# Kernel tuning notes

Hardware: AMD Instinct MI355X
Metric: run time of the kernel (lower is better)

Reference implementation:

```python
import jax, jax.numpy as jnp
import numpy as np
import math

V, L, D, H, S_MAX = 32000, 6, 768, 8, 256
HD = D // H
SCALE_FACTOR = 2  # attn_scale_factor in the original (TUPE-style)
POS_SCALING = float(HD * SCALE_FACTOR) ** (-0.5)
REL_BINS, MAX_DIST = 32, 128


def _rel_pos_bucket_np(rel, num_buckets=REL_BINS, max_distance=MAX_DIST):
    # bidirectional T5-style bucketing (faithful to relative_position_bucket)
    n = -rel
    num_buckets //= 2
    ret = (n < 0).astype(np.int64) * num_buckets
    n = np.abs(n)
    max_exact = num_buckets // 2
    is_small = n < max_exact
    val_if_large = max_exact + (
        np.log(np.maximum(n, 1).astype(np.float32) / max_exact)
        / math.log(max_distance / max_exact) * (num_buckets - max_exact)
    ).astype(np.int64)
    val_if_large = np.minimum(val_if_large, num_buckets - 1)
    ret += np.where(is_small, n, val_if_large)
    return ret


def _layernorm(x, g, b, eps=1e-5):
    mu = jnp.mean(x, axis=-1, keepdims=True)
    var = jnp.var(x, axis=-1, keepdims=True)
    return (x - mu) * jax.lax.rsqrt(var + eps) * g + b


def setup_inputs() -> dict:
    key = jax.random.key(0)
    ks = jax.random.split(key, 16)
    B, S = 32, 256
    init = lambda k, shape: (jax.random.normal(k, shape, jnp.float32) * 0.02)
    pos_idx = np.arange(S)
    rp = _rel_pos_bucket_np(pos_idx[None, :] - pos_idx[:, None])  # [S,S]
    return {
        "tokens": jax.random.randint(ks[0], (B, S), 0, V, dtype=jnp.int32),
        "embed_tokens": init(ks[1], (V, D)),
        "pos_emb": init(ks[2], (S_MAX + 1, D)),
        "pos_q_w": init(ks[3], (D, D)), "pos_q_b": jnp.zeros((D,), jnp.float32),
        "pos_k_w": init(ks[4], (D, D)), "pos_k_b": jnp.zeros((D,), jnp.float32),
        "pos_ln_g": jnp.ones((D,), jnp.float32), "pos_ln_b": jnp.zeros((D,), jnp.float32),
        "rel_bias_table": init(ks[5], (REL_BINS + 1, H)),
        "rp_bucket": jnp.asarray(rp, jnp.int32),
        "Wq": init(ks[6], (L, D, D)), "bq": jnp.zeros((L, D), jnp.float32),
        "Wk": init(ks[7], (L, D, D)), "bk": jnp.zeros((L, D), jnp.float32),
        "Wv": init(ks[8], (L, D, D)), "bv": jnp.zeros((L, D), jnp.float32),
        "Wo": init(ks[9], (L, D, D)), "bo": jnp.zeros((L, D), jnp.float32),
    }


def reference(tokens, embed_tokens, pos_emb, pos_q_w, pos_q_b, pos_k_w, pos_k_b,
              pos_ln_g, pos_ln_b, rel_bias_table, rp_bucket,
              Wq, bq, Wk, bk, Wv, bv, Wo, bo):
    B, S = tokens.shape
    # relative positional bias: bucket lookup -> [H,S,S]
    rel_bias = rel_bias_table[rp_bucket]            # [S,S,H]
    rel_bias = jnp.transpose(rel_bias, (2, 0, 1))   # [H,S,S]
    # absolute positional bias (TUPE): LN(pos) -> per-head q/k -> bmm
    w = _layernorm(pos_emb[:S], pos_ln_g, pos_ln_b)             # [S,D]
    pq = (w @ pos_q_w.T + pos_q_b).reshape(S, H, HD) * POS_SCALING
    pk = (w @ pos_k_w.T + pos_k_b).reshape(S, H, HD)
    abs_bias = jnp.einsum('ihd,jhd->hij', pq, pk)               # [H,S,S]
    bias = (abs_bias + rel_bias)[None]                          # [1,H,S,S]

    x = embed_tokens[tokens]                                    # [B,S,D]
    scale = float(HD * SCALE_FACTOR) ** (-0.5)
    for l in range(L):
        q = (x @ Wq[l].T + bq[l]).reshape(B, S, H, HD) * scale
        k = (x @ Wk[l].T + bk[l]).reshape(B, S, H, HD)
        v = (x @ Wv[l].T + bv[l]).reshape(B, S, H, HD)
        scores = jnp.einsum('bihd,bjhd->bhij', q, k) + bias     # [B,H,S,S]
        attn = jax.nn.softmax(scores, axis=-1)
        o = jnp.einsum('bhij,bjhd->bihd', attn, v).reshape(B, S, D)
        x = o @ Wo[l].T + bo[l]
    return x[:, 0, :]  # sentence rep [B,D]
```

## Files before the change

### kernel.cpp

```cpp
#include <hip/hip_runtime.h>
#include <hip/hip_bf16.h>
#include <math.h>

constexpr int SEQ = 256;
constexpr int DIM = 768;
constexpr int NH  = 8;
constexpr int HD  = 96;

typedef __attribute__((ext_vector_type(8))) short short8;
typedef __attribute__((ext_vector_type(4))) float f32x4;
using bf16 = __hip_bfloat16;

#define ASYNC_COPY16(gptr, lptr) \
  __builtin_amdgcn_global_load_lds((const __attribute__((address_space(1))) void*)(gptr), \
                                   (__attribute__((address_space(3))) void*)(lptr), 16, 0, 0)

__global__ __launch_bounds__(256) void gemm_kernel(
    const float* __restrict__ A, int lda, long aoz,
    const float* __restrict__ W, int ldw, long woz,
    const float* __restrict__ bias, long boz,
    bf16* __restrict__ C, int ldc, long coz,
    int M, int N, int K, float scale,
    const int* __restrict__ rp, const float* __restrict__ rtab)
{
    const int hz = blockIdx.z;
    A += (long)hz * aoz;
    W += (long)hz * woz;
    if (bias) bias += (long)hz * boz;
    C += (long)hz * coz;

    __shared__ float As[16][68];
    __shared__ float Ws[16][68];

    const int bm = blockIdx.y * 64;
    const int bn = blockIdx.x * 64;
    const int tid = threadIdx.x;
    const int tx = tid & 15;
    const int ty = tid >> 4;

    float acc[4][4] = {};

    for (int k0 = 0; k0 < K; k0 += 16) {
#pragma unroll
        for (int i = 0; i < 4; i++) {
            int idx = tid + i * 256;
            int r = idx >> 4, c = idx & 15;
            As[c][r] = A[(long)(bm + r) * lda + (k0 + c)];
            Ws[c][r] = W[(long)(bn + r) * ldw + (k0 + c)];
        }
        __syncthreads();
#pragma unroll
        for (int kk = 0; kk < 16; kk++) {
            const float4 a = *(const float4*)&As[kk][ty * 4];
            const float4 w = *(const float4*)&Ws[kk][tx * 4];
            acc[0][0] += a.x * w.x; acc[0][1] += a.x * w.y; acc[0][2] += a.x * w.z; acc[0][3] += a.x * w.w;
            acc[1][0] += a.y * w.x; acc[1][1] += a.y * w.y; acc[1][2] += a.y * w.z; acc[1][3] += a.y * w.w;
            acc[2][0] += a.z * w.x; acc[2][1] += a.z * w.y; acc[2][2] += a.z * w.z; acc[2][3] += a.z * w.w;
            acc[3][0] += a.w * w.x; acc[3][1] += a.w * w.y; acc[3][2] += a.w * w.z; acc[3][3] += a.w * w.w;
        }
        __syncthreads();
    }

    const int n0 = bn + tx * 4;
    float4 bv = make_float4(0.f, 0.f, 0.f, 0.f);
    if (bias) bv = *(const float4*)&bias[n0];
#pragma unroll
    for (int i = 0; i < 4; i++) {
        const int m = bm + ty * 4 + i;
        float4 r;
        if (rtab) {
            r.x = acc[i][0] * scale + rtab[rp[(n0 + 0) * 256 + m] * 8 + hz];
            r.y = acc[i][1] * scale + rtab[rp[(n0 + 1) * 256 + m] * 8 + hz];
            r.z = acc[i][2] * scale + rtab[rp[(n0 + 2) * 256 + m] * 8 + hz];
            r.w = acc[i][3] * scale + rtab[rp[(n0 + 3) * 256 + m] * 8 + hz];
        } else {
            r.x = (acc[i][0] + bv.x) * scale;
            r.y = (acc[i][1] + bv.y) * scale;
            r.z = (acc[i][2] + bv.z) * scale;
            r.w = (acc[i][3] + bv.w) * scale;
        }
        bf16 t4[4];
        t4[0] = __float2bfloat16(r.x);
        t4[1] = __float2bfloat16(r.y);
        t4[2] = __float2bfloat16(r.z);
        t4[3] = __float2bfloat16(r.w);
        *(uint2*)&C[(long)m * ldc + n0] = *(uint2*)t4;
    }
}

constexpr int RB_A = 10368;
constexpr int RB_B = RB_A + 3456;
constexpr int RB_C = RB_B + 54;
constexpr int RB_D = RB_C + 6144;
constexpr int RB_E = RB_D + 256;
constexpr int RB_F = RB_E + 1152;
constexpr int RB_G = RB_F + 2;

__global__ __launch_bounds__(256) void setup_mega_kernel(
    const int* __restrict__ tokens, const float* __restrict__ embed,
    const float* __restrict__ pos_emb,
    const float* __restrict__ pos_q_w, const float* __restrict__ pos_q_b,
    const float* __restrict__ pos_k_w, const float* __restrict__ pos_k_b,
    const float* __restrict__ pos_ln_g, const float* __restrict__ pos_ln_b,
    const float* __restrict__ Wq, const float* __restrict__ Wk,
    const float* __restrict__ Wv, const float* __restrict__ Wo,
    const float* __restrict__ bq, const float* __restrict__ bk,
    const float* __restrict__ bv,
    bf16* __restrict__ wqkv, bf16* __restrict__ woT, float* __restrict__ bqkv,
    bf16* __restrict__ xb, bf16* __restrict__ wln,
    bf16* __restrict__ wsW, float* __restrict__ wsB, float scale)
{
    const int bid = blockIdx.x, tid = threadIdx.x;

    if (bid < RB_A) {
        const long idx = (long)bid * 256 + tid;
        const long e = idx * 4;
        const int k = (int)(e % 768);
        const long nl = e / 768;
        const int n = (int)(nl % 2304);
        const int l = (int)(nl / 2304);
        const float* src;
        float sc = 1.f;
        if (n < 768)       { src = Wq + ((long)l * 768 + n) * 768; sc = scale; }
        else if (n < 1536) { src = Wk + ((long)l * 768 + (n - 768)) * 768; }
        else               { src = Wv + ((long)l * 768 + (n - 1536)) * 768; }
        const float4 v = *(const float4*)&src[k];
        bf16 tmp[4];
        tmp[0] = __float2bfloat16(v.x * sc);
        tmp[1] = __float2bfloat16(v.y * sc);
        tmp[2] = __float2bfloat16(v.z * sc);
        tmp[3] = __float2bfloat16(v.w * sc);
        *(uint2*)&wqkv[((long)l * 2304 + n) * 768 + k] = *(uint2*)tmp;
    } else if (bid < RB_B) {
        __shared__ float t[32][33];
        const int b2 = bid - RB_A;
        const int l = b2 / 576, r2 = b2 % 576;
        const int c0 = (r2 % 24) * 32, j0 = (r2 / 24) * 32;
        const int tx = tid & 31, ty = tid >> 5;
        const float* src = Wo + (long)l * 768 * 768;
#pragma unroll
        for (int rr = 0; rr < 32; rr += 8)
            t[ty + rr][tx] = src[(long)(c0 + ty + rr) * 768 + j0 + tx];
        __syncthreads();
        bf16* dst = woT + (long)l * 768 * 768;
#pragma unroll
        for (int rr = 0; rr < 32; rr += 8)
            dst[(long)(j0 + ty + rr) * 768 + c0 + tx] = __float2bfloat16(t[tx][ty + rr]);
    } else if (bid < RB_C) {
        const int idx = (bid - RB_B) * 256 + tid;
        if (idx < 6 * 2304) {
            const int n = idx % 2304, l = idx / 2304;
            float v;
            if (n < 768)       v = bq[l * 768 + n] * scale;
            else if (n < 1536) v = bk[l * 768 + (n - 768)];
            else               v = bv[l * 768 + (n - 1536)];
            bqkv[idx] = v;
        }
    } else if (bid < RB_D) {
        const int idx = (bid - RB_C) * 256 + tid;
        const int t = idx / 192;
        const int d = idx - t * 192;
        const int tok = tokens[t];
        const float4 v = ((const float4*)(embed + (long)tok * DIM))[d];
        bf16 tmp[4];
        tmp[0] = __float2bfloat16(v.x);
        tmp[1] = __float2bfloat16(v.y);
        tmp[2] = __float2bfloat16(v.z);
        tmp[3] = __float2bfloat16(v.w);
        *(uint2*)&xb[(long)t * DIM + d * 4] = *(uint2*)tmp;
    } else if (bid < RB_E) {
        __shared__ float buf[256];
        const int i = bid - RB_D;
        const float* row = pos_emb + (long)i * DIM;
        float v0 = row[tid], v1 = row[tid + 256], v2 = row[tid + 512];
        buf[tid] = v0 + v1 + v2;
        __syncthreads();
        for (int off = 128; off > 0; off >>= 1) {
            if (tid < off) buf[tid] += buf[tid + off];
            __syncthreads();
        }
        const float mean = buf[0] * (1.f / 768.f);
        __syncthreads();
        const float d0 = v0 - mean, d1 = v1 - mean, d2 = v2 - mean;
        buf[tid] = d0 * d0 + d1 * d1 + d2 * d2;
        __syncthreads();
        for (int off = 128; off > 0; off >>= 1) {
            if (tid < off) buf[tid] += buf[tid + off];
            __syncthreads();
        }
        const float rstd = rsqrtf(buf[0] * (1.f / 768.f) + 1e-5f);
        bf16* wr = wln + (long)i * DIM;
        wr[tid]       = __float2bfloat16(d0 * rstd * pos_ln_g[tid]       + pos_ln_b[tid]);
        wr[tid + 256] = __float2bfloat16(d1 * rstd * pos_ln_g[tid + 256] + pos_ln_b[tid + 256]);
        wr[tid + 512] = __float2bfloat16(d2 * rstd * pos_ln_g[tid + 512] + pos_ln_b[tid + 512]);
    } else if (bid < RB_F) {
        const long idx = (long)(bid - RB_E) * 256 + tid;
        const long e = idx * 4;
        const float4 v = (e < 589824) ? *(const float4*)&pos_q_w[e]
                                      : *(const float4*)&pos_k_w[e - 589824];
        bf16 tmp[4];
        tmp[0] = __float2bfloat16(v.x);
        tmp[1] = __float2bfloat16(v.y);
        tmp[2] = __float2bfloat16(v.z);
        tmp[3] = __float2bfloat16(v.w);
        *(uint2*)&wsW[e] = *(uint2*)tmp;
    } else {
        const int idx = (bid - RB_F) * 256 + tid;
        wsB[idx] = (idx < 768) ? pos_q_b[idx] : pos_k_b[idx - 768];
    }
}

__global__ __launch_bounds__(256) void fused_bias_kernel(
    const bf16* __restrict__ wqkv, const float* __restrict__ bo,
    const float* __restrict__ bqkv, float* __restrict__ bf_)
{
    const int l = blockIdx.y;
    const int lane = threadIdx.x & 63, wave = threadIdx.x >> 6;
    const int nloc = wave * 8 + (lane >> 3);
    const int seg = lane & 7;
    const int n = blockIdx.x * 32 + nloc;
    const bf16* wrow = wqkv + ((long)(l + 1) * 2304 + n) * 768 + seg * 96;
    const float* bsrc = bo + (long)l * 768 + seg * 96;
    float s = 0.f;
#pragma unroll
    for (int c8 = 0; c8 < 12; c8++) {
        const short8 w8 = *(const short8*)&wrow[c8 * 8];
#pragma unroll
        for (int e = 0; e < 8; e++) {
            bf16 b;
            *(short*)&b = w8[e];
            s += __bfloat162float(b) * bsrc[c8 * 8 + e];
        }
    }
    s += __shfl_xor(s, 1);
    s += __shfl_xor(s, 2);
    s += __shfl_xor(s, 4);
    if (seg == 0) bf_[l * 2304 + n] = s + bqkv[(l + 1) * 2304 + n];
}

#define GEMM_PREF(AS, BS, KB)                                                 \
  {                                                                           \
    _Pragma("unroll")                                                         \
    for (int i = 0; i < 2; i++) {                                             \
      const int u = tid + i * 512;                                            \
      const int r = u >> 3, c = u & 7;                                        \
      const int ca = c ^ (r & 7);                                             \
      ASYNC_COPY16(A + (bm + r) * (long)K + (KB) + ca * 8, &AS[u * 8]);       \
      ASYNC_COPY16(B + (bn + r) * (long)K + (KB) + ca * 8, &BS[u * 8]);       \
    }                                                                         \
  }

#define GEMM_COMPUTE(AS, BS)                                                  \
  {                                                                           \
    _Pragma("unroll")                                                         \
    for (int ks = 0; ks < 2; ks++) {                                          \
      const int cc = ks * 4 + quad;                                           \
      short8 af[4], bfr[2];                                                   \
      _Pragma("unroll")                                                       \
      for (int t = 0; t < 4; t++) {                                           \
        const int ra = wm * 64 + t * 16 + col;                                \
        af[t] = *(const short8*)&AS[ra * 64 + ((cc ^ (ra & 7)) * 8)];         \
      }                                                                       \
      _Pragma("unroll")                                                       \
      for (int t = 0; t < 2; t++) {                                           \
        const int rb = wn * 32 + t * 16 + col;                                \
        bfr[t] = *(const short8*)&BS[rb * 64 + ((cc ^ (rb & 7)) * 8)];        \
      }                                                                       \
      _Pragma("unroll")                                                       \
      for (int tm = 0; tm < 4; tm++)                                          \
        _Pragma("unroll")                                                     \
        for (int tn = 0; tn < 2; tn++)                                        \
          acc[tm][tn] = __builtin_amdgcn_mfma_f32_16x16x32_bf16(af[tm], bfr[tn], acc[tm][tn], 0, 0, 0); \
    }                                                                         \
  }

__global__ __launch_bounds__(512, 4) void gemm_bf16_kernel(
    const bf16* __restrict__ A, const bf16* __restrict__ B,
    const float* __restrict__ bias,
    bf16* __restrict__ Cb, bf16* __restrict__ vTout, float* __restrict__ Cf,
    int N, int K, int swz, long az, long bz, long cz, long biasz, int skipQ)
{
    __shared__ bf16 As0[128 * 64];
    __shared__ bf16 Bs0[128 * 64];
    __shared__ bf16 As1[128 * 64];
    __shared__ bf16 Bs1[128 * 64];

    A += (long)blockIdx.z * az;
    B += (long)blockIdx.z * bz;
    if (Cb) Cb += (long)blockIdx.z * cz;
    if (Cf) Cf += (long)blockIdx.z * cz;
    if (bias) bias += (long)blockIdx.z * biasz;

    const int tid = threadIdx.x;
    const int lane = tid & 63, wave = tid >> 6;
    const int wm = wave & 1, wn = wave >> 1;

    int bmt, bnt;
    if (swz) {
        const int id = blockIdx.x + gridDim.x * blockIdx.y;
        const int xcd = id & 7, loc = id >> 3;
        bmt = xcd * 8 + (loc & 7);
        bnt = loc >> 3;
    } else {
        bmt = blockIdx.y;
        bnt = blockIdx.x;
    }
    if (skipQ && bnt < 6 && (bmt & 1)) return;

    const long bm = (long)bmt * 128, bn = (long)bnt * 128;
    const int col = lane & 15, quad = lane >> 4;

    f32x4 acc[4][2] = {};

    GEMM_PREF(As0, Bs0, 0);
    for (int kk = 0; kk < K; kk += 128) {
        __syncthreads();
        GEMM_PREF(As1, Bs1, kk + 64);
        GEMM_COMPUTE(As0, Bs0);
        __syncthreads();
        if (kk + 128 < K) GEMM_PREF(As0, Bs0, kk + 128);
        GEMM_COMPUTE(As1, Bs1);
    }

    const bool toVT = (vTout != nullptr) && (bn >= 1536);

    if (toVT) {
        __syncthreads();
        bf16* tb = (wave < 4 ? As0 : Bs0) + (wave & 3) * 2048;
#pragma unroll
        for (int tn = 0; tn < 2; tn++) {
            const int nl = tn * 16 + col;
            const float bvv = bias[bn + wn * 32 + nl];
#pragma unroll
            for (int tm = 0; tm < 4; tm++) {
                const int mc = tm * 4 + quad;
                bf16 t4[4];
#pragma unroll
                for (int r = 0; r < 4; r++)
                    t4[r] = __float2bfloat16(acc[tm][tn][r] + bvv);
                *(uint2*)&tb[(nl * 16 + (mc ^ (nl & 15))) * 4] = *(uint2*)t4;
            }
        }
        const int b_  = (int)((bm + wm * 64) >> 8);
        const int s0  = (int)((bm + wm * 64) & 255);
        const long nb = bn + wn * 32 - 1536;
#pragma unroll
        for (int it2 = 0; it2 < 8; it2++) {
            const int nl = it2 * 4 + quad;
            const uint2 v = *(const uint2*)&tb[(nl * 16 + (col ^ (nl & 15))) * 4];
            *(uint2*)&vTout[((long)b_ * 768 + nb + nl) * 256 + s0 + col * 4] = v;
        }
    } else if (Cf) {
#pragma unroll
        for (int tn = 0; tn < 2; tn++) {
            const long n = bn + wn * 32 + tn * 16 + col;
            const float bvv = bias ? bias[n] : 0.f;
#pragma unroll
            for (int tm = 0; tm < 4; tm++) {
                const long m0 = bm + wm * 64 + tm * 16 + quad * 4;
#pragma unroll
                for (int r = 0; r < 4; r++)
                    Cf[(m0 + r) * N + n] = acc[tm][tn][r] + bvv;
            }
        }
    } else {
#pragma unroll
        for (int tn = 0; tn < 2; tn++) {
            const long n = bn + wn * 32 + tn * 16 + col;
            const float bvv = bias ? bias[n] : 0.f;
#pragma unroll
            for (int tm = 0; tm < 4; tm++) {
                const long m0 = bm + wm * 64 + tm * 16 + quad * 4;
#pragma unroll
                for (int r = 0; r < 4; r++)
                    Cb[(m0 + r) * N + n] = __float2bfloat16(acc[tm][tn][r] + bvv);
            }
        }
    }
}

#define PREF_K(DST, JC)                                                      \
  { _Pragma("unroll")                                                        \
    for (int i = 0; i < 4; i++) {                                            \
      const int u = tid + i * 256;                                           \
      const int r = u >> 4, pp = u & 15;                                     \
      const int c = pp ^ (r & 15);                                           \
      ASYNC_COPY16(kbase + ((JC) * 64 + r) * 2304 + c * 8, &DST[u * 8]);     \
    } }

#define PREF_V(DST, KC)                                                      \
  { _Pragma("unroll")                                                        \
    for (int i = 0; i < 3; i++) {                                            \
      const int u = tid + i * 256;                                           \
      const int r = u >> 3, pp = u & 7;                                      \
      const int c = pp ^ (r & 7);                                            \
      ASYNC_COPY16(vbase + r * 256 + (KC) * 64 + c * 8, &DST[u * 8]);        \
    } }

#define SCORE(BUF, JC)                                                       \
  { _Pragma("unroll")                                                        \
    for (int ks = 0; ks < 3; ks++) {                                         \
      _Pragma("unroll")                                                      \
      for (int jt2 = 0; jt2 < 4; jt2++) {                                    \
        const int row = jt2 * 16 + col;                                      \
        const int c = ks * 4 + quad;                                         \
        const short8 bk_ = *(const short8*)&BUF[row * 128 + ((c ^ (row & 15)) * 8)]; \
        accS[(JC) * 4 + jt2] = __builtin_amdgcn_mfma_f32_16x16x32_bf16(aq[ks], bk_, accS[(JC) * 4 + jt2], 0, 0, 0); \
      } } }

#define PV(BUF, KC)                                                          \
  { _Pragma("unroll")                                                        \
    for (int k2 = 0; k2 < 2; k2++) {                                         \
      const short8 ap = *(const short8*)&Ps[(wave * 16 + col) * PS + (KC) * 64 + k2 * 32 + quad * 8]; \
      _Pragma("unroll")                                                      \
      for (int nt = 0; nt < 6; nt++) {                                       \
        const int row = nt * 16 + col;                                       \
        const int c = k2 * 4 + quad;                                         \
        const short8 bv_ = *(const short8*)&BUF[row * 64 + ((c ^ (row & 7)) * 8)]; \
        accO[nt] = __builtin_amdgcn_mfma_f32_16x16x32_bf16(ap, bv_, accO[nt], 0, 0, 0); \
      } } }

__global__ __launch_bounds__(256) void attn_mfma_kernel(
    const bf16* __restrict__ qkv, const bf16* __restrict__ vT,
    const bf16* __restrict__ biasT, bf16* __restrict__ o)
{
    constexpr int PS = 264;
    __shared__ bf16 Ps[64 * PS];
    __shared__ bf16 KV0[64 * 128];
    __shared__ bf16 KV1[64 * 128];

    const int blk = blockIdx.x;
    const int b  = blk & 31;
    const int h  = (blk >> 5) & 7;
    const int it = blk >> 8;
    const int i0 = it * 64;
    const int tid = threadIdx.x, lane = tid & 63, wave = tid >> 6;
    const int col = lane & 15, quad = lane >> 4;
    const long rowbase = (long)b * SEQ;

    const bf16* kbase = qkv + rowbase * 2304 + 768 + h * 96;
    const bf16* vbase = vT + ((long)b * 768 + h * 96) * 256;

    PREF_K(KV0, 0);

    short8 aq[3];
    {
        const bf16* qrow = qkv + (rowbase + i0 + wave * 16 + col) * 2304 + h * 96;
#pragma unroll
        for (int ks = 0; ks < 3; ks++)
            aq[ks] = *(const short8*)&qrow[ks * 32 + quad * 8];
    }

    f32x4 accS[16] = {};
    __syncthreads();
    PREF_K(KV1, 1);
    SCORE(KV0, 0);
    __syncthreads();
    PREF_K(KV0, 2);
    SCORE(KV1, 1);
    __syncthreads();
    PREF_K(KV1, 3);
    SCORE(KV0, 2);
    __syncthreads();
    PREF_V(KV0, 0);
    SCORE(KV1, 3);

    const bf16* bbT = biasT + (long)h * SEQ * SEQ + i0 + wave * 16 + quad * 4;
#pragma unroll
    for (int jt = 0; jt < 16; jt++) {
        bf16 b4[4];
        *(uint2*)b4 = *(const uint2*)&bbT[(long)(jt * 16 + col) * SEQ];
        accS[jt][0] += __bfloat162float(b4[0]);
        accS[jt][1] += __bfloat162float(b4[1]);
        accS[jt][2] += __bfloat162float(b4[2]);
        accS[jt][3] += __bfloat162float(b4[3]);
    }

#pragma unroll
    for (int r = 0; r < 4; r++) {
        float m = accS[0][r];
#pragma unroll
        for (int jt = 1; jt < 16; jt++) m = fmaxf(m, accS[jt][r]);
        for (int d = 1; d < 16; d <<= 1) m = fmaxf(m, __shfl_xor(m, d));
        float s = 0.f;
#pragma unroll
        for (int jt = 0; jt < 16; jt++) {
            const float e = __expf(accS[jt][r] - m);
            accS[jt][r] = e;
            s += e;
        }
        for (int d = 1; d < 16; d <<= 1) s += __shfl_xor(s, d);
        const float inv = 1.f / s;
        const int prow = wave * 16 + quad * 4 + r;
#pragma unroll
        for (int jt = 0; jt < 16; jt++)
            Ps[prow * PS + jt * 16 + col] = __float2bfloat16(accS[jt][r] * inv);
    }

    f32x4 accO[6] = {};
    __syncthreads();
    PREF_V(KV1, 1);
    PV(KV0, 0);
    __syncthreads();
    PREF_V(KV0, 2);
    PV(KV1, 1);
    __syncthreads();
    PREF_V(KV1, 3);
    PV(KV0, 2);
    __syncthreads();
    PV(KV1, 3);

#pragma unroll
    for (int nt = 0; nt < 6; nt++)
#pragma unroll
        for (int r = 0; r < 4; r++) {
            const long m = rowbase + i0 + wave * 16 + quad * 4 + r;
            o[m * DIM + h * 96 + nt * 16 + col] = __float2bfloat16(accO[nt][r]);
        }
}

__global__ __launch_bounds__(256) void final_out_kernel(
    const bf16* __restrict__ ob, const float* __restrict__ Wo5,
    const float* __restrict__ bo5, float* __restrict__ out)
{
    __shared__ float os[768];
    const int b = blockIdx.y, ng = blockIdx.x, tid = threadIdx.x;
    const bf16* orow = ob + (long)b * 256 * 768;
    for (int i = tid; i < 768; i += 256) os[i] = __bfloat162float(orow[i]);
    __syncthreads();

    const int n = ng * 32 + (tid >> 3);
    const int seg = tid & 7;
    const float* wrow = Wo5 + (long)n * 768 + seg * 96;
    const float* xs = &os[seg * 96];
    float s = 0.f;
#pragma unroll
    for (int k = 0; k < 96; k += 4) {
        const float4 w = *(const float4*)&wrow[k];
        s += xs[k] * w.x + xs[k + 1] * w.y + xs[k + 2] * w.z + xs[k + 3] * w.w;
    }
    s += __shfl_xor(s, 1);
    s += __shfl_xor(s, 2);
    s += __shfl_xor(s, 4);
    if (seg == 0) out[b * 768 + n] = s + bo5[n];
}

extern "C" void kernel_launch(void* const* d_in, const int* in_sizes, int n_in,
                              void* d_out, int out_size, void* d_ws, size_t ws_size,
                              hipStream_t stream)
{
    const int*   tokens   = (const int*)d_in[0];
    const float* embed    = (const float*)d_in[1];
    const float* pos_emb  = (const float*)d_in[2];
    const float* pos_q_w  = (const float*)d_in[3];
    const float* pos_q_b  = (const float*)d_in[4];
    const float* pos_k_w  = (const float*)d_in[5];
    const float* pos_k_b  = (const float*)d_in[6];
    const float* pos_ln_g = (const float*)d_in[7];
    const float* pos_ln_b = (const float*)d_in[8];
    const float* rel_tab  = (const float*)d_in[9];
    const int*   rp       = (const int*)d_in[10];
    const float* Wq = (const float*)d_in[11];
    const float* bq = (const float*)d_in[12];
    const float* Wk = (const float*)d_in[13];
    const float* bk = (const float*)d_in[14];
    const float* Wv = (const float*)d_in[15];
    const float* bv = (const float*)d_in[16];
    const float* Wo = (const float*)d_in[17];
    const float* bo = (const float*)d_in[18];
    float* out = (float*)d_out;

    char* p = (char*)d_ws;
    auto alloc = [&](size_t bytes) -> char* {
        char* r = p;
        p += (bytes + 255) & ~(size_t)255;
        return r;
    };
    const long NT = 32L * SEQ;

    bf16*  biasT = (bf16*) alloc(8L * SEQ * SEQ * 2);
    bf16*  wlnb  = (bf16*) alloc((long)SEQ * DIM * 2);
    float* pqk   = (float*)alloc(2L * SEQ * DIM * 4);
    bf16*  wsWb  = (bf16*) alloc(2L * 768 * 768 * 2);
    float* wsB   = (float*)alloc(2L * 768 * 4);
    bf16*  xb    = (bf16*) alloc(NT * DIM * 2);
    bf16*  qkv   = (bf16*) alloc(NT * 2304 * 2);
    bf16*  vT    = (bf16*) alloc(NT * DIM * 2);
    bf16*  ob    = (bf16*) alloc(NT * DIM * 2);
    bf16*  wqkv  = (bf16*) alloc(6L * 2304 * 768 * 2);
    bf16*  woT   = (bf16*) alloc(6L * 768 * 768 * 2);
    bf16*  wf    = (bf16*) alloc(5L * 2304 * 768 * 2);
    float* bqkv  = (float*)alloc(6L * 2304 * 4);
    float* bfus  = (float*)alloc(5L * 2304 * 4);

    const float SCALE = 0.07216878364870322f;

    setup_mega_kernel<<<RB_G, 256, 0, stream>>>(
        tokens, embed, pos_emb, pos_q_w, pos_q_b, pos_k_w, pos_k_b,
        pos_ln_g, pos_ln_b, Wq, Wk, Wv, Wo, bq, bk, bv,
        wqkv, woT, bqkv, xb, wlnb, wsWb, wsB, SCALE);

    gemm_bf16_kernel<<<dim3(6, 18, 5), 512, 0, stream>>>(
        wqkv + 2304L * 768, woT, nullptr, wf, nullptr, nullptr, 768, 768, 0,
        2304L * 768, 768L * 768, 2304L * 768, 0, 0);
    fused_bias_kernel<<<dim3(72, 5), 256, 0, stream>>>(wqkv, bo, bqkv, bfus);

    gemm_bf16_kernel<<<dim3(6, 2, 2), 512, 0, stream>>>(
        wlnb, wsWb, wsB, nullptr, nullptr, pqk, 768, 768, 0,
        0, 768L * 768, (long)SEQ * DIM, 768, 0);
    gemm_kernel<<<dim3(4, 4, NH), 256, 0, stream>>>(
        pqk + (long)SEQ * DIM, DIM, HD, pqk, DIM, HD, nullptr, 0,
        biasT, SEQ, (long)SEQ * SEQ, SEQ, SEQ, HD, SCALE, rp, rel_tab);

    gemm_bf16_kernel<<<dim3(18, 64, 1), 512, 0, stream>>>(
        xb, wqkv, bqkv, qkv, vT, nullptr, 2304, 768, 1, 0, 0, 0, 0, 0);
    for (int l = 0; l < 5; l++) {
        attn_mfma_kernel<<<1024, 256, 0, stream>>>(qkv, vT, biasT, ob);
        gemm_bf16_kernel<<<dim3(18, 64, 1), 512, 0, stream>>>(
            ob, wf + (long)l * 2304 * 768, bfus + (long)l * 2304, qkv, vT, nullptr,
            2304, 768, 1, 0, 0, 0, 0, (l == 4) ? 1 : 0);
    }
    attn_mfma_kernel<<<256, 256, 0, stream>>>(qkv, vT, biasT, ob);
    final_out_kernel<<<dim3(24, 32), 256, 0, stream>>>(ob, Wo + 5L * 768 * 768, bo + 5L * 768, out);
}
```

Baseline: 640.0 us.

## Halve attention P buffer, raise occupancy, add MFMA priority and head-major block order

The softmax probability tile in shared memory shrinks to half its width. The second half of the probabilities stays in registers and is written only after the first two PV chunks have consumed the first half. Launch bounds now request 4 blocks per CU, MFMA sections are wrapped in s_setprio, block index decoding becomes head-fastest so blocks sharing a batch's K/V run together, and the max and reciprocal reductions are restructured. Keeping accS live longer raises register pressure under the tighter launch bound, and reusing the Ps buffer depends on the barrier placement being correct.

Result: slower. 653.1 us (+2.0%).

```diff
diff --git a/kernel.cpp b/kernel.cpp
--- a/kernel.cpp
+++ b/kernel.cpp
@@ -398,7 +398,8 @@
     } }
 
 #define SCORE(BUF, JC)                                                       \
-  { _Pragma("unroll")                                                        \
+  { __builtin_amdgcn_s_setprio(1);                                           \
+    _Pragma("unroll")                                                        \
     for (int ks = 0; ks < 3; ks++) {                                         \
       _Pragma("unroll")                                                      \
       for (int jt2 = 0; jt2 < 4; jt2++) {                                    \
@@ -406,32 +407,35 @@
         const int c = ks * 4 + quad;                                         \
         const short8 bk_ = *(const short8*)&BUF[row * 128 + ((c ^ (row & 15)) * 8)]; \
         accS[(JC) * 4 + jt2] = __builtin_amdgcn_mfma_f32_16x16x32_bf16(aq[ks], bk_, accS[(JC) * 4 + jt2], 0, 0, 0); \
-      } } }
-
-#define PV(BUF, KC)                                                          \
-  { _Pragma("unroll")                                                        \
+      } }                                                                     \
+    __builtin_amdgcn_s_setprio(0); }
+
+#define PV(BUF, PC)                                                          \
+  { __builtin_amdgcn_s_setprio(1);                                           \
+    _Pragma("unroll")                                                        \
     for (int k2 = 0; k2 < 2; k2++) {                                         \
-      const short8 ap = *(const short8*)&Ps[(wave * 16 + col) * PS + (KC) * 64 + k2 * 32 + quad * 8]; \
+      const short8 ap = *(const short8*)&Ps[(wave * 16 + col) * PS + (PC) * 64 + k2 * 32 + quad * 8]; \
       _Pragma("unroll")                                                      \
       for (int nt = 0; nt < 6; nt++) {                                       \
         const int row = nt * 16 + col;                                       \
         const int c = k2 * 4 + quad;                                         \
         const short8 bv_ = *(const short8*)&BUF[row * 64 + ((c ^ (row & 7)) * 8)]; \
         accO[nt] = __builtin_amdgcn_mfma_f32_16x16x32_bf16(ap, bv_, accO[nt], 0, 0, 0); \
-      } } }
-
-__global__ __launch_bounds__(256) void attn_mfma_kernel(
+      } }                                                                     \
+    __builtin_amdgcn_s_setprio(0); }
+
+__global__ __launch_bounds__(256, 4) void attn_mfma_kernel(
     const bf16* __restrict__ qkv, const bf16* __restrict__ vT,
     const bf16* __restrict__ biasT, bf16* __restrict__ o)
 {
-    constexpr int PS = 264;
+    constexpr int PS = 136;
     __shared__ bf16 Ps[64 * PS];
     __shared__ bf16 KV0[64 * 128];
     __shared__ bf16 KV1[64 * 128];
 
     const int blk = blockIdx.x;
-    const int b  = blk & 31;
-    const int h  = (blk >> 5) & 7;
+    const int h  = blk & 7;
+    const int b  = (blk >> 3) & 31;
     const int it = blk >> 8;
     const int i0 = it * 64;
     const int tid = threadIdx.x, lane = tid & 63, wave = tid >> 6;
@@ -478,9 +482,12 @@
 
 #pragma unroll
     for (int r = 0; r < 4; r++) {
-        float m = accS[0][r];
-#pragma unroll
-        for (int jt = 1; jt < 16; jt++) m = fmaxf(m, accS[jt][r]);
+        float t0 = fmaxf(fmaxf(accS[0][r],  accS[1][r]),  accS[2][r]);
+        float t1 = fmaxf(fmaxf(accS[3][r],  accS[4][r]),  accS[5][r]);
+        float t2 = fmaxf(fmaxf(accS[6][r],  accS[7][r]),  accS[8][r]);
+        float t3 = fmaxf(fmaxf(accS[9][r],  accS[10][r]), accS[11][r]);
+        float t4 = fmaxf(fmaxf(accS[12][r], accS[13][r]), accS[14][r]);
+        float m  = fmaxf(fmaxf(fmaxf(t0, t1), t2), fmaxf(fmaxf(t3, t4), accS[15][r]));
         for (int d = 1; d < 16; d <<= 1) m = fmaxf(m, __shfl_xor(m, d));
         float s = 0.f;
 #pragma unroll
@@ -490,11 +497,13 @@
             s += e;
         }
         for (int d = 1; d < 16; d <<= 1) s += __shfl_xor(s, d);
-        const float inv = 1.f / s;
+        const float inv = __builtin_amdgcn_rcpf(s);
+#pragma unroll
+        for (int jt = 0; jt < 16; jt++) accS[jt][r] *= inv;
         const int prow = wave * 16 + quad * 4 + r;
 #pragma unroll
-        for (int jt = 0; jt < 16; jt++)
-            Ps[prow * PS + jt * 16 + col] = __float2bfloat16(accS[jt][r] * inv);
+        for (int jt = 0; jt < 8; jt++)
+            Ps[prow * PS + jt * 16 + col] = __float2bfloat16(accS[jt][r]);
     }
 
     f32x4 accO[6] = {};
@@ -504,11 +513,18 @@
     __syncthreads();
     PREF_V(KV0, 2);
     PV(KV1, 1);
+#pragma unroll
+    for (int r = 0; r < 4; r++) {
+        const int prow = wave * 16 + quad * 4 + r;
+#pragma unroll
+        for (int jt = 8; jt < 16; jt++)
+            Ps[prow * PS + (jt - 8) * 16 + col] = __float2bfloat16(accS[jt][r]);
+    }
     __syncthreads();
     PREF_V(KV1, 3);
-    PV(KV0, 2);
-    __syncthreads();
-    PV(KV1, 3);
+    PV(KV0, 0);
+    __syncthreads();
+    PV(KV1, 1);
 
 #pragma unroll
     for (int nt = 0; nt < 6; nt++)
```
